# Kernel tuning notes

Hardware: AMD Instinct MI355X
Metric: run time of the kernel (lower is better)

## Reference

```python
import jax, jax.numpy as jnp
import numpy as np

B, S, D = 2048, 200, 128   # batch, n_steps, embedding dim per vector
H = 64                      # hidden_dim
MASK_SCALE = 1e10


def setup_inputs() -> dict:
    key = jax.random.key(0)
    ks = jax.random.split(key, 6)
    his = jax.random.normal(ks[0], (B, S, D), dtype=jnp.float32)
    target = jax.random.normal(ks[1], (B, 1, D), dtype=jnp.float32)
    # mask == 1.0 marks padded history positions (they get -1e10 added pre-softmax)
    mask = (jax.random.uniform(ks[2], (B, S)) < 0.3).astype(jnp.float32)
    W = jax.random.normal(ks[3], (3 * D, H), dtype=jnp.float32) * 0.1
    W_bias = jnp.full((H,), 0.1, dtype=jnp.float32)
    O = jax.random.normal(ks[4], (H, 1), dtype=jnp.float32) * 0.1
    O_bias = jnp.full((1,), 0.1, dtype=jnp.float32)
    return {"his": his, "target": target, "mask": mask,
            "W": W, "W_bias": W_bias, "O": O, "O_bias": O_bias}


def reference(his, target, mask, W, W_bias, O, O_bias):
    tgt = jnp.broadcast_to(target, his.shape)          # [B,S,D] tile over steps
    diff = his - tgt
    att_vec = jnp.concatenate([his, diff, tgt], axis=2)  # [B,S,3D]
    h = jax.nn.relu(jnp.einsum('bsf,fh->bsh', att_vec, W) + W_bias)  # [B,S,H]
    alpha = jnp.einsum('bsh,ho->bso', h, O) + O_bias   # [B,S,1]
    alpha = alpha[:, :, 0] - mask * MASK_SCALE         # [B,S]
    attn = jax.nn.softmax(alpha, axis=-1)              # [B,S]
    out = jnp.einsum('bs,bsd->bd', attn, his)          # weighted-sum pooling
    return out
```

## Files before the change

kernel.cpp:

```cpp
#include <hip/hip_runtime.h>

#define B_ 2048
#define S_ 200
#define D_ 128
#define H_ 64
#define MASK_SCALE 1e10f
#define LSTRIDE 136

typedef __attribute__((ext_vector_type(8))) short short8_t;
typedef __attribute__((ext_vector_type(4))) float f32x4;
typedef __attribute__((ext_vector_type(4))) unsigned short ushort4_t;

__device__ __forceinline__ unsigned short f2bf(float f) {
    unsigned u = __float_as_uint(f);
    unsigned r = (u + 0x7fffu + ((u >> 16) & 1u)) >> 16;
    return (unsigned short)r;
}
__device__ __forceinline__ float bf2f(unsigned short v) {
    return __uint_as_float(((unsigned)v) << 16);
}

__global__ __launch_bounds__(256) void prep_w(const float* __restrict__ W,
                                              float* __restrict__ wt,
                                              unsigned short* __restrict__ wfrag) {
    for (int idx = threadIdx.x; idx < D_ * H_; idx += 256) {
        int d = idx >> 6;
        int h = idx & 63;
        float w1 = W[d * H_ + h];
        float w2 = W[(D_ + d) * H_ + h];
        float w3 = W[(2 * D_ + d) * H_ + h];
        wt[idx] = w3 - w2;
        int kt = d >> 5, q = (d >> 3) & 3, j = d & 7;
        int nt = h >> 4, lm = h & 15;
        int lane = (q << 4) | lm;
        wfrag[((kt * 4 + nt) * 64 + lane) * 8 + j] = f2bf(w1 + w2);
    }
}

__global__ __launch_bounds__(64) void prep_tproj(const float* __restrict__ target,
                                                 const float* __restrict__ W_bias,
                                                 const float* __restrict__ wt,
                                                 float* __restrict__ tproj) {
    int b = blockIdx.x;
    int h = threadIdx.x;
    float acc = W_bias[h];
    const float* tg = target + (size_t)b * D_;
    #pragma unroll 8
    for (int d = 0; d < D_; ++d)
        acc = fmaf(tg[d], wt[d * H_ + h], acc);
    tproj[b * H_ + h] = acc;
}

__global__ __launch_bounds__(256, 2) void fused_kernel(const float* __restrict__ his,
                                                       const float* __restrict__ mask,
                                                       const unsigned short* __restrict__ wfrag,
                                                       const float* __restrict__ tproj,
                                                       const float* __restrict__ Ovec,
                                                       float* __restrict__ out) {
    __shared__ unsigned short hisb[S_ * LSTRIDE];
    __shared__ float alpha_s[208];
    __shared__ float red8[8];
    __shared__ float tp_s[H_];
    __shared__ float ov_s[H_];
    __shared__ float pool_s[3 * D_];

    const int b    = blockIdx.x;
    const int t    = threadIdx.x;
    const int lane = t & 63;
    const int wv   = t >> 6;
    const int lm   = lane & 15;
    const int q    = lane >> 4;

    short8_t bfrag[16];
    #pragma unroll
    for (int f = 0; f < 16; ++f)
        bfrag[f] = *(const short8_t*)(wfrag + ((size_t)(f * 64 + lane)) * 8);

    if (t < H_) {
        tp_s[t] = tproj[b * H_ + t];
        ov_s[t] = Ovec[t];
    }

    const float4* hb4 = (const float4*)(his + (size_t)b * S_ * D_);
    #pragma unroll
    for (int i = t, it = 0; it < (S_ * D_ / 4 + 255) / 256; ++it, i += 256) {
        if (i < S_ * D_ / 4) {
            float4 x = hb4[i];
            int s  = i >> 5;
            int d4 = i & 31;
            ushort4_t v;
            v[0] = f2bf(x.x); v[1] = f2bf(x.y); v[2] = f2bf(x.z); v[3] = f2bf(x.w);
            *(ushort4_t*)(&hisb[s * LSTRIDE + d4 * 4]) = v;
        }
    }
    __syncthreads();

    for (int tile = wv; tile < 13; tile += 4) {
        int row0 = tile * 16;
        int ar = row0 + lm; if (ar > S_ - 1) ar = S_ - 1;
        const unsigned short* ap = &hisb[ar * LSTRIDE + q * 8];

        f32x4 acc[4];
        #pragma unroll
        for (int nt = 0; nt < 4; ++nt) acc[nt] = (f32x4){0.f, 0.f, 0.f, 0.f};

        #pragma unroll
        for (int kt = 0; kt < 4; ++kt) {
            short8_t a = *(const short8_t*)(ap + kt * 32);
            #pragma unroll
            for (int nt = 0; nt < 4; ++nt)
                acc[nt] = __builtin_amdgcn_mfma_f32_16x16x32_bf16(a, bfrag[kt * 4 + nt], acc[nt], 0, 0, 0);
        }

        float part[4];
        #pragma unroll
        for (int r = 0; r < 4; ++r) {
            float sum = 0.f;
            #pragma unroll
            for (int nt = 0; nt < 4; ++nt) {
                int h = nt * 16 + lm;
                float v = acc[nt][r] + tp_s[h];
                v = fmaxf(v, 0.f);
                sum = fmaf(v, ov_s[h], sum);
            }
            part[r] = sum;
        }
        #pragma unroll
        for (int off = 1; off < 16; off <<= 1) {
            #pragma unroll
            for (int r = 0; r < 4; ++r)
                part[r] += __shfl_xor(part[r], off);
        }
        if (lm == 0) {
            #pragma unroll
            for (int r = 0; r < 4; ++r)
                alpha_s[row0 + q * 4 + r] = part[r];
        }
    }
    __syncthreads();

    float a = (t < S_) ? alpha_s[t] - mask[(size_t)b * S_ + t] * MASK_SCALE : -INFINITY;
    float m = a;
    #pragma unroll
    for (int off = 1; off < 64; off <<= 1) m = fmaxf(m, __shfl_xor(m, off));
    if (lane == 0) red8[wv] = m;
    __syncthreads();
    m = fmaxf(fmaxf(red8[0], red8[1]), fmaxf(red8[2], red8[3]));
    float e = (t < S_) ? __expf(a - m) : 0.f;
    float ssum = e;
    #pragma unroll
    for (int off = 1; off < 64; off <<= 1) ssum += __shfl_xor(ssum, off);
    if (lane == 0) red8[4 + wv] = ssum;
    __syncthreads();
    float inv = 1.f / (red8[4] + red8[5] + red8[6] + red8[7]);
    __syncthreads();
    if (t < S_) alpha_s[t] = e * inv;
    __syncthreads();

    const int d2 = t & 63;
    const int sg = t >> 6;
    float ax = 0.f, ay = 0.f;
    for (int s = sg; s < S_; s += 4) {
        float w = alpha_s[s];
        unsigned v = *(const unsigned*)(&hisb[s * LSTRIDE + d2 * 2]);
        ax = fmaf(w, bf2f((unsigned short)(v & 0xffff)), ax);
        ay = fmaf(w, bf2f((unsigned short)(v >> 16)), ay);
    }
    if (sg) {
        pool_s[(sg - 1) * D_ + d2 * 2]     = ax;
        pool_s[(sg - 1) * D_ + d2 * 2 + 1] = ay;
    }
    __syncthreads();
    if (sg == 0) {
        #pragma unroll
        for (int k = 0; k < 3; ++k) {
            ax += pool_s[k * D_ + d2 * 2];
            ay += pool_s[k * D_ + d2 * 2 + 1];
        }
        float2 o; o.x = ax; o.y = ay;
        ((float2*)out)[b * (D_ / 2) + d2] = o;
    }
}

extern "C" void kernel_launch(void* const* d_in, const int* in_sizes, int n_in,
                              void* d_out, int out_size, void* d_ws, size_t ws_size,
                              hipStream_t stream) {
    const float* his    = (const float*)d_in[0];
    const float* target = (const float*)d_in[1];
    const float* mask   = (const float*)d_in[2];
    const float* W      = (const float*)d_in[3];
    const float* W_bias = (const float*)d_in[4];
    const float* Ovec   = (const float*)d_in[5];
    float* out = (float*)d_out;

    char* ws = (char*)d_ws;
    float* wt             = (float*)(ws);
    unsigned short* wfrag = (unsigned short*)(ws + 32768);
    float* tproj          = (float*)(ws + 65536);

    prep_w<<<1, 256, 0, stream>>>(W, wt, wfrag);
    prep_tproj<<<B_, 64, 0, stream>>>(target, W_bias, wt, tproj);
    fused_kernel<<<B_, 256, 0, stream>>>(his, mask, wfrag, tproj, Ovec, out);
}
```

Baseline: 328.2 us.

## Fuse target projection into main kernel and drop LDS row padding

Removes the separate prep_tproj launch. One wave of each block now computes the per-batch target projection directly from W while the other three waves convert the history tile to bf16 in LDS. prep_w is spread over 32 blocks. The LDS row padding is removed, which lets occupancy rise to 3 blocks per CU, but it may bring back bank conflicts on the MFMA A-fragment reads. The mask load is hoisted to the start and the pooling now uses 4-wide vector loads plus a shuffle reduction.

```diff
diff --git a/kernel.cpp b/kernel.cpp
--- a/kernel.cpp
+++ b/kernel.cpp
@@ -5,7 +5,6 @@
 #define D_ 128
 #define H_ 64
 #define MASK_SCALE 1e10f
-#define LSTRIDE 136
 
 typedef __attribute__((ext_vector_type(8))) short short8_t;
 typedef __attribute__((ext_vector_type(4))) float f32x4;
@@ -21,43 +20,27 @@
 }
 
 __global__ __launch_bounds__(256) void prep_w(const float* __restrict__ W,
-                                              float* __restrict__ wt,
                                               unsigned short* __restrict__ wfrag) {
-    for (int idx = threadIdx.x; idx < D_ * H_; idx += 256) {
-        int d = idx >> 6;
-        int h = idx & 63;
-        float w1 = W[d * H_ + h];
-        float w2 = W[(D_ + d) * H_ + h];
-        float w3 = W[(2 * D_ + d) * H_ + h];
-        wt[idx] = w3 - w2;
-        int kt = d >> 5, q = (d >> 3) & 3, j = d & 7;
-        int nt = h >> 4, lm = h & 15;
-        int lane = (q << 4) | lm;
-        wfrag[((kt * 4 + nt) * 64 + lane) * 8 + j] = f2bf(w1 + w2);
-    }
+    int idx = blockIdx.x * 256 + threadIdx.x;
+    int d = idx >> 6;
+    int h = idx & 63;
+    float w1 = W[d * H_ + h];
+    float w2 = W[(D_ + d) * H_ + h];
+    int kt = d >> 5, q = (d >> 3) & 3, j = d & 7;
+    int nt = h >> 4, lm = h & 15;
+    int lane = (q << 4) | lm;
+    wfrag[((kt * 4 + nt) * 64 + lane) * 8 + j] = f2bf(w1 + w2);
 }
 
-__global__ __launch_bounds__(64) void prep_tproj(const float* __restrict__ target,
-                                                 const float* __restrict__ W_bias,
-                                                 const float* __restrict__ wt,
-                                                 float* __restrict__ tproj) {
-    int b = blockIdx.x;
-    int h = threadIdx.x;
-    float acc = W_bias[h];
-    const float* tg = target + (size_t)b * D_;
-    #pragma unroll 8
-    for (int d = 0; d < D_; ++d)
-        acc = fmaf(tg[d], wt[d * H_ + h], acc);
-    tproj[b * H_ + h] = acc;
-}
-
-__global__ __launch_bounds__(256, 2) void fused_kernel(const float* __restrict__ his,
+__global__ __launch_bounds__(256, 3) void fused_kernel(const float* __restrict__ his,
+                                                       const float* __restrict__ target,
                                                        const float* __restrict__ mask,
+                                                       const float* __restrict__ W,
+                                                       const float* __restrict__ W_bias,
+                                                       const float* __restrict__ Ovec,
                                                        const unsigned short* __restrict__ wfrag,
-                                                       const float* __restrict__ tproj,
-                                                       const float* __restrict__ Ovec,
                                                        float* __restrict__ out) {
-    __shared__ unsigned short hisb[S_ * LSTRIDE];
+    __shared__ unsigned short hisb[S_ * D_];
     __shared__ float alpha_s[208];
     __shared__ float red8[8];
     __shared__ float tp_s[H_];
@@ -71,34 +54,40 @@
     const int lm   = lane & 15;
     const int q    = lane >> 4;
 
+    float mk = (t < S_) ? mask[(size_t)b * S_ + t] : 0.f;
+
     short8_t bfrag[16];
     #pragma unroll
     for (int f = 0; f < 16; ++f)
         bfrag[f] = *(const short8_t*)(wfrag + ((size_t)(f * 64 + lane)) * 8);
 
-    if (t < H_) {
-        tp_s[t] = tproj[b * H_ + t];
-        ov_s[t] = Ovec[t];
-    }
-
-    const float4* hb4 = (const float4*)(his + (size_t)b * S_ * D_);
-    #pragma unroll
-    for (int i = t, it = 0; it < (S_ * D_ / 4 + 255) / 256; ++it, i += 256) {
-        if (i < S_ * D_ / 4) {
+    if (wv < 3) {
+        const float4* hb4 = (const float4*)(his + (size_t)b * S_ * D_);
+        const int tid3 = wv * 64 + lane;
+        for (int i = tid3; i < S_ * D_ / 4; i += 192) {
             float4 x = hb4[i];
-            int s  = i >> 5;
-            int d4 = i & 31;
             ushort4_t v;
             v[0] = f2bf(x.x); v[1] = f2bf(x.y); v[2] = f2bf(x.z); v[3] = f2bf(x.w);
-            *(ushort4_t*)(&hisb[s * LSTRIDE + d4 * 4]) = v;
+            *(ushort4_t*)(&hisb[i * 4]) = v;
         }
+    } else {
+        const float* tg = target + (size_t)b * D_;
+        float acc = W_bias[lane];
+        #pragma unroll 4
+        for (int d = 0; d < D_; ++d) {
+            float w2 = W[(D_ + d) * H_ + lane];
+            float w3 = W[(2 * D_ + d) * H_ + lane];
+            acc = fmaf(tg[d], w3 - w2, acc);
+        }
+        tp_s[lane] = acc;
+        ov_s[lane] = Ovec[lane];
     }
     __syncthreads();
 
     for (int tile = wv; tile < 13; tile += 4) {
         int row0 = tile * 16;
         int ar = row0 + lm; if (ar > S_ - 1) ar = S_ - 1;
-        const unsigned short* ap = &hisb[ar * LSTRIDE + q * 8];
+        const unsigned short* ap = &hisb[ar * D_ + q * 8];
 
         f32x4 acc[4];
         #pragma unroll
@@ -139,7 +128,7 @@
     }
     __syncthreads();
 
-    float a = (t < S_) ? alpha_s[t] - mask[(size_t)b * S_ + t] * MASK_SCALE : -INFINITY;
+    float a = (t < S_) ? alpha_s[t] - mk * MASK_SCALE : -INFINITY;
     float m = a;
     #pragma unroll
     for (int off = 1; off < 64; off <<= 1) m = fmaxf(m, __shfl_xor(m, off));
@@ -157,28 +146,34 @@
     if (t < S_) alpha_s[t] = e * inv;
     __syncthreads();
 
-    const int d2 = t & 63;
-    const int sg = t >> 6;
-    float ax = 0.f, ay = 0.f;
-    for (int s = sg; s < S_; s += 4) {
+    const int d4 = t & 31;
+    const int sg = t >> 5;
+    float acc0 = 0.f, acc1 = 0.f, acc2 = 0.f, acc3 = 0.f;
+    for (int s = sg; s < S_; s += 8) {
         float w = alpha_s[s];
-        unsigned v = *(const unsigned*)(&hisb[s * LSTRIDE + d2 * 2]);
-        ax = fmaf(w, bf2f((unsigned short)(v & 0xffff)), ax);
-        ay = fmaf(w, bf2f((unsigned short)(v >> 16)), ay);
+        ushort4_t v = *(const ushort4_t*)(&hisb[s * D_ + d4 * 4]);
+        acc0 = fmaf(w, bf2f(v[0]), acc0);
+        acc1 = fmaf(w, bf2f(v[1]), acc1);
+        acc2 = fmaf(w, bf2f(v[2]), acc2);
+        acc3 = fmaf(w, bf2f(v[3]), acc3);
     }
-    if (sg) {
-        pool_s[(sg - 1) * D_ + d2 * 2]     = ax;
-        pool_s[(sg - 1) * D_ + d2 * 2 + 1] = ay;
+    acc0 += __shfl_xor(acc0, 32);
+    acc1 += __shfl_xor(acc1, 32);
+    acc2 += __shfl_xor(acc2, 32);
+    acc3 += __shfl_xor(acc3, 32);
+    if (wv && lane < 32) {
+        float4 p; p.x = acc0; p.y = acc1; p.z = acc2; p.w = acc3;
+        *(float4*)(&pool_s[(wv - 1) * D_ + d4 * 4]) = p;
     }
     __syncthreads();
-    if (sg == 0) {
+    if (wv == 0 && lane < 32) {
         #pragma unroll
         for (int k = 0; k < 3; ++k) {
-            ax += pool_s[k * D_ + d2 * 2];
-            ay += pool_s[k * D_ + d2 * 2 + 1];
+            const float4 p = *(const float4*)(&pool_s[k * D_ + d4 * 4]);
+            acc0 += p.x; acc1 += p.y; acc2 += p.z; acc3 += p.w;
         }
-        float2 o; o.x = ax; o.y = ay;
-        ((float2*)out)[b * (D_ / 2) + d2] = o;
+        float4 o; o.x = acc0; o.y = acc1; o.z = acc2; o.w = acc3;
+        *(float4*)(out + (size_t)b * D_ + d4 * 4) = o;
     }
 }
 
@@ -193,12 +188,8 @@
     const float* Ovec   = (const float*)d_in[5];
     float* out = (float*)d_out;
 
-    char* ws = (char*)d_ws;
-    float* wt             = (float*)(ws);
-    unsigned short* wfrag = (unsigned short*)(ws + 32768);
-    float* tproj          = (float*)(ws + 65536);
+    unsigned short* wfrag = (unsigned short*)d_ws;
 
-    prep_w<<<1, 256, 0, stream>>>(W, wt, wfrag);
-    prep_tproj<<<B_, 64, 0, stream>>>(target, W_bias, wt, tproj);
-    fused_kernel<<<B_, 256, 0, stream>>>(his, mask, wfrag, tproj, Ovec, out);
+    prep_w<<<32, 256, 0, stream>>>(W, wfrag);
+    fused_kernel<<<B_, 256, 0, stream>>>(his, target, mask, W, W_bias, Ovec, wfrag, out);
 }
```

Measured after the change: 347.6 us. 5.9% more time.
